# Kernel optimization log

Measured on AMD Instinct MI355X. Metric: run time of the kernel, lower is better.

Reference implementation:

```python
import jax, jax.numpy as jnp
import numpy as np

NEG_SLOPE = 0.2   # LeakyReLU default negative slope (GATv2 + nn.LeakyReLU)
K_NEIGH = 16      # att_args['num_neighs']


def leaky(x):
    return jnp.where(x >= 0, x, NEG_SLOPE * x)


def knn_idx(x_feat, y_feat, k):
    """Per-batch KNN of y in x (feature space). x_feat,y_feat: [B,M,C] -> [B,M,k] local idx into x."""
    d = (jnp.sum(y_feat * y_feat, -1, keepdims=True)
         - 2.0 * jnp.einsum('bmc,bnc->bmn', y_feat, x_feat)
         + jnp.sum(x_feat * x_feat, -1)[:, None, :])   # [B,M,M]
    _, idx = jax.lax.top_k(-d, k)
    return idx


def gatv2_bipartite(x_last, x_past, nbr, Wl, Wr, att_w):
    """Faithful GATv2Conv((last, past), edge_index) with flow='target_to_source',
    heads H, concat=False (mean over heads), bias=False, no self loops.
    x_j = lin_l(x[0]=last) gathered at knn neighbor (col) indices,
    x_i = lin_r(x[1]=past) at query (row) indices; each query has exactly K edges."""
    N, C = x_last.shape
    H = att_w.shape[0]
    xl = (x_last @ Wl).reshape(N, H, C)          # [N,H,C]
    xr = (x_past @ Wr).reshape(N, H, C)          # [N,H,C]
    xlj = xl[nbr]                                 # [N,K,H,C] gathered source msgs
    e = jnp.einsum('nkhc,hc->nkh', leaky(xlj + xr[:, None]), att_w)  # [N,K,H]
    a = jax.nn.softmax(e, axis=1)                 # softmax over each target's K edges
    out = jnp.einsum('nkh,nkhc->nhc', a, xlj)     # [N,H,C]
    return out.mean(axis=1)                       # concat=False -> head mean, [N,C]


def reference(pc_encoded_seq, W1, b1, W2, b2, Wl, Wr, att_w, batch_size, m_points):
    T, N, C = pc_encoded_seq.shape
    B, M = batch_size, m_points
    G = W2.shape[1]
    # node_level_proj (Linear-LeakyReLU-Linear-LeakyReLU) + global_mean_pool per frame
    h = leaky(leaky(pc_encoded_seq @ W1 + b1) @ W2 + b2)      # [T,N,G]
    global_fea = h.reshape(T, B, M, G).mean(axis=2)            # [T,B,G]
    # frame-level ScaledDotProductAttention: q = last frame, k=v = past frames
    q = global_fea[-1][:, None, :]                             # [B,1,G]
    kv = jnp.transpose(global_fea[:-1], (1, 0, 2))             # [B,T-1,G]
    score = jnp.einsum('bqg,btg->bqt', q, kv) / jnp.sqrt(jnp.asarray(G, jnp.float32))
    attn = jax.nn.softmax(score, axis=-1)                      # [B,1,T-1]
    last = pc_encoded_seq[-1]                                  # [N,C]
    lastb = last.reshape(B, M, C)
    offs = (jnp.arange(B) * M)[:, None, None]
    res = []
    for i in range(T - 1):   # small fixed frame count
        past = pc_encoded_seq[i]
        nbr = knn_idx(past.reshape(B, M, C), lastb, K_NEIGH) + offs  # global idx
        out = gatv2_bipartite(last, past, nbr.reshape(N, K_NEIGH), Wl, Wr, att_w)
        res.append(out.reshape(B, M, C))
    res = jnp.stack(res, axis=1)                               # [B,T-1,M,C]
    fw = attn[:, 0, :, None, None]                             # [B,T-1,1,1]
    weighted = jnp.sum(res * fw, axis=1)                       # [B,M,C]
    tm_out = jnp.concatenate([last, weighted.reshape(N, C)], axis=-1)  # [N,2C]
    return tm_out


def setup_inputs() -> dict:
    key = jax.random.key(0)
    ks = jax.random.split(key, 8)
    T, B, M, C, G, H = 5, 4, 4096, 128, 1024, 4
    N = B * M
    s = lambda fan: 1.0 / np.sqrt(fan)
    return {
        'pc_encoded_seq': jax.random.normal(ks[0], (T, N, C), jnp.float32),
        'W1': jax.random.normal(ks[1], (C, 128), jnp.float32) * s(C),
        'b1': jnp.zeros((128,), jnp.float32),
        'W2': jax.random.normal(ks[2], (128, G), jnp.float32) * s(128),
        'b2': jnp.zeros((G,), jnp.float32),
        'Wl': jax.random.normal(ks[3], (C, H * C), jnp.float32) * s(C),
        'Wr': jax.random.normal(ks[4], (C, H * C), jnp.float32) * s(C),
        'att_w': jax.random.normal(ks[5], (H, C), jnp.float32) * s(C),
        'batch_size': B,
        'm_points': M,
    }
```

## Files before the change

### kernel.cpp

```cpp
#include <hip/hip_runtime.h>
#include <hip/hip_bf16.h>
#include <hip/hip_fp16.h>


typedef __bf16 v8bf __attribute__((ext_vector_type(8)));
typedef float  v4f  __attribute__((ext_vector_type(4)));

__device__ __forceinline__ float lrelu(float x) { return fmaxf(x, 0.2f * x); }

__device__ __forceinline__ unsigned short f2bf(float x) {
  __hip_bfloat16 h = __float2bfloat16(x);
  return __builtin_bit_cast(unsigned short, h);
}
__device__ __forceinline__ float bf2f(unsigned short u) {
  unsigned int t = ((unsigned int)u) << 16;
  return __builtin_bit_cast(float, t);
}

#define GLOAD_LDS16(gp, lp)                                                   \
  __builtin_amdgcn_global_load_lds(                                           \
      (const __attribute__((address_space(1))) void*)(gp),                    \
      (__attribute__((address_space(3))) void*)(lp), 16, 0, 0)

#define RBAR() do { __builtin_amdgcn_s_barrier(); asm volatile("" ::: "memory"); } while (0)
#define LWAIT() do { asm volatile("s_waitcnt lgkmcnt(0)" ::: "memory");        \
                     __builtin_amdgcn_sched_barrier(0); } while (0)

template<int EP>
__global__ __launch_bounds__(256, 2)
void nt_mfma(const unsigned short* __restrict__ A, const unsigned short* __restrict__ B,
             const float* __restrict__ aux, void* __restrict__ outv, int K, int ldc)
{
  __shared__ __align__(16) unsigned short smem[3 * 8192];
  const int tid = threadIdx.x;
  const int l = tid & 63;
  const int w = tid >> 6;
  const int wm = w & 1, wn = w >> 1;
  const int m0 = blockIdx.y << 7, n0 = blockIdx.x << 7;
  const int fr = l & 15, quad = l >> 4;
  const int kt = K >> 5;
  const int xq4 = quad ^ ((fr >> 1) & 3);

  const int r0 = tid >> 2;
  const int sw = (tid & 3) ^ ((tid >> 3) & 3);
  const unsigned short* Aa = A + (size_t)(m0 + r0) * K + sw * 8;
  const unsigned short* Ab = Aa + (size_t)64 * K;
  const unsigned short* Ba = B + (size_t)(n0 + r0) * K + sw * 8;
  const unsigned short* Bb = Ba + (size_t)64 * K;

  auto stage = [&](int bi, int ks) {
    unsigned short* As = smem + bi * 8192;
    unsigned short* Bs = As + 4096;
    GLOAD_LDS16(Aa + ks * 32, As + tid * 8);
    GLOAD_LDS16(Ab + ks * 32, As + (tid + 256) * 8);
    GLOAD_LDS16(Ba + ks * 32, Bs + tid * 8);
    GLOAD_LDS16(Bb + ks * 32, Bs + (tid + 256) * 8);
  };

  v4f acc[4][4];
#pragma unroll
  for (int i = 0; i < 4; ++i)
#pragma unroll
    for (int j = 0; j < 4; ++j) acc[i][j] = (v4f){0.f, 0.f, 0.f, 0.f};

  stage(0, 0);
  if (kt > 1) stage(1, 1);
  int cur = 0, pend = (kt > 1) ? 2 : 1, sn = 2;

  for (int ks = 0; ks < kt; ++ks) {
    if (pend == 2) asm volatile("s_waitcnt vmcnt(4)" ::: "memory");
    else           asm volatile("s_waitcnt vmcnt(0)" ::: "memory");
    RBAR();
    int nb = cur + 2; if (nb >= 3) nb -= 3;
    if (sn < kt) { stage(nb, sn); ++sn; } else { --pend; }
    const unsigned short* As = smem + cur * 8192;
    const unsigned short* Bs = As + 4096;
    v8bf af[4], bfr[4];
#pragma unroll
    for (int i = 0; i < 4; ++i)
      af[i] = *(const v8bf*)(As + (wm * 64 + i * 16 + fr) * 32 + xq4 * 8);
#pragma unroll
    for (int j = 0; j < 4; ++j)
      bfr[j] = *(const v8bf*)(Bs + (wn * 64 + j * 16 + fr) * 32 + xq4 * 8);
#pragma unroll
    for (int i = 0; i < 4; ++i)
#pragma unroll
      for (int j = 0; j < 4; ++j)
        acc[i][j] = __builtin_amdgcn_mfma_f32_16x16x32_bf16(af[i], bfr[j], acc[i][j], 0, 0, 0);
    __builtin_amdgcn_sched_barrier(0);
    if (++cur == 3) cur = 0;
  }

  if (EP == 1) {
    unsigned short* O = (unsigned short*)outv;
#pragma unroll
    for (int j = 0; j < 4; ++j) {
      int col = n0 + wn * 64 + j * 16 + fr;
      float bias = aux[col];
#pragma unroll
      for (int i = 0; i < 4; ++i) {
        int row = m0 + wm * 64 + i * 16 + quad * 4;
#pragma unroll
        for (int r = 0; r < 4; ++r)
          O[(size_t)(row + r) * ldc + col] = f2bf(lrelu(acc[i][j][r] + bias));
      }
    }
  } else if (EP == 2) {
    __syncthreads();
    float* red = (float*)smem;
#pragma unroll
    for (int j = 0; j < 4; ++j) {
      int lcol = wn * 64 + j * 16 + fr;
      float bias = aux[n0 + lcol];
      float s = 0.f;
#pragma unroll
      for (int i = 0; i < 4; ++i)
#pragma unroll
        for (int r = 0; r < 4; ++r) s += lrelu(acc[i][j][r] + bias);
      s += __shfl_xor(s, 16);
      s += __shfl_xor(s, 32);
      if (quad == 0) red[w * 128 + lcol] = s;
    }
    __syncthreads();
    if (tid < 128) {
      float s = (tid < 64) ? red[0 * 128 + tid] + red[1 * 128 + tid]
                           : red[2 * 128 + tid] + red[3 * 128 + tid];
      atomicAdd((float*)outv + ((m0 >> 12) << 10) + n0 + tid, s * (1.0f / 4096.0f));
    }
  } else {
    __half* O = (__half*)outv;
#pragma unroll
    for (int j = 0; j < 4; ++j) {
      int col = n0 + wn * 64 + j * 16 + fr;
#pragma unroll
      for (int i = 0; i < 4; ++i) {
        int row = m0 + wm * 64 + i * 16 + quad * 4;
#pragma unroll
        for (int r = 0; r < 4; ++r)
          O[(size_t)(row + r) * ldc + col] = __float2half(acc[i][j][r]);
      }
    }
  }
}

#define TOPN 24
#define TSTR 25
#define FB   16
#define PSTR 17

__global__ __launch_bounds__(256, 2)
void knn_coarse(const unsigned short* __restrict__ seqbf,
                const float* __restrict__ xsq, int* __restrict__ candOut)
{
  __shared__ __align__(16) unsigned short smem[16384];
  __shared__ float topV[128 * TSTR];
  __shared__ int   topI[128 * TSTR];
  __shared__ float pushV[128 * PSTR];
  __shared__ int   pushI[128 * PSTR];
  __shared__ int   cntW[128];

  const int tid = threadIdx.x;
  const int l = tid & 63;
  const int w = tid >> 6;
  const int pair = blockIdx.x >> 5;
  const int rb = blockIdx.x & 31;
  const int f = pair >> 2, b = pair & 3;
  const int m0 = rb << 7;
  const int fr = l & 15, quad = l >> 4;
  const int xq4 = quad ^ ((fr >> 1) & 3);

  const unsigned short* ybase = seqbf + ((size_t)65536 + b * 4096) * 128;
  const unsigned short* xbase = seqbf + ((size_t)(f * 16384 + b * 4096)) * 128;
  const float* xq = xsq + f * 16384 + b * 4096;

  const int r0 = tid >> 2;
  const int sw = (tid & 3) ^ ((tid >> 3) & 3);

#pragma unroll
  for (int kk = 0; kk < 4; ++kk) {
    const unsigned short* Ag = ybase + (size_t)(m0 + r0) * 128 + kk * 32 + sw * 8;
    GLOAD_LDS16(Ag, smem + kk * 4096 + tid * 8);
    GLOAD_LDS16(Ag + 64 * 128, smem + kk * 4096 + (tid + 256) * 8);
  }
  asm volatile("s_waitcnt vmcnt(0)" ::: "memory");
  RBAR();

  v8bf afr[4][2];
#pragma unroll
  for (int kk = 0; kk < 4; ++kk)
#pragma unroll
    for (int i = 0; i < 2; ++i)
      afr[kk][i] = *(const v8bf*)(smem + kk * 4096 + (w * 32 + i * 16 + fr) * 32 + xq4 * 8);
  LWAIT();

  float tauReg = -3.0e38f;
  float ownMin = -3.0e38f;
  int   ownMinPos = 0;
  if (l < 32) {
    const int grow = w * 32 + l;
#pragma unroll
    for (int k = 0; k < TOPN; ++k) { topV[grow * TSTR + k] = -3.0e38f; topI[grow * TSTR + k] = k; }
    cntW[grow] = 0;
  }
  float tc[8];
#pragma unroll
  for (int i = 0; i < 8; ++i) tc[i] = -3.0e38f;

  for (int ct = 0; ct < 32; ++ct) {
    const int n0 = ct << 7;
    RBAR();
    {
      const unsigned short* Bt = xbase + (size_t)(n0 + r0) * 128 + sw * 8;
#pragma unroll
      for (int kk = 0; kk < 4; ++kk) {
        GLOAD_LDS16(Bt + kk * 32, smem + kk * 4096 + tid * 8);
        GLOAD_LDS16(Bt + 64 * 128 + kk * 32, smem + kk * 4096 + (tid + 256) * 8);
      }
    }
    float xsv[8];
#pragma unroll
    for (int j = 0; j < 8; ++j) xsv[j] = xq[n0 + j * 16 + fr];
    asm volatile("s_waitcnt vmcnt(0)" ::: "memory");
    RBAR();

    v4f acc[2][8];
#pragma unroll
    for (int i = 0; i < 2; ++i)
#pragma unroll
      for (int j = 0; j < 8; ++j) acc[i][j] = (v4f){0.f, 0.f, 0.f, 0.f};

#pragma unroll
    for (int ksp = 0; ksp < 4; ++ksp) {
      v8bf bfr[8];
#pragma unroll
      for (int j = 0; j < 8; ++j)
        bfr[j] = *(const v8bf*)(smem + ksp * 4096 + (j * 16 + fr) * 32 + xq4 * 8);
#pragma unroll
      for (int i = 0; i < 2; ++i)
#pragma unroll
        for (int j = 0; j < 8; ++j)
          acc[i][j] = __builtin_amdgcn_mfma_f32_16x16x32_bf16(afr[ksp][i], bfr[j], acc[i][j], 0, 0, 0);
    }

#pragma unroll
    for (int i = 0; i < 2; ++i)
#pragma unroll
      for (int j = 0; j < 8; ++j)
#pragma unroll
        for (int r = 0; r < 4; ++r)
          acc[i][j][r] = 2.f * acc[i][j][r] - xsv[j];

    if (ct == 0) {
#pragma unroll
      for (int i = 0; i < 2; ++i)
#pragma unroll
        for (int r = 0; r < 4; ++r) {
          float t1 = fmaxf(acc[i][0][r], acc[i][1][r]);
          float t2 = fminf(acc[i][0][r], acc[i][1][r]);
#pragma unroll
          for (int j = 2; j < 8; ++j) {
            float v = acc[i][j][r];
            float hi = fmaxf(t1, v);
            t2 = fmaxf(t2, fminf(t1, v));
            t1 = hi;
          }
#pragma unroll
          for (int off = 1; off <= 8; off <<= 1)
            t2 = fminf(t2, __shfl_xor(t2, off));
          tc[i * 4 + r] = t2;
          float tq = __shfl(t2, (((l >> 2) & 3) << 4));
          if (l < 32 && (l >> 4) == i && (l & 3) == r) tauReg = tq;
        }
    }

    unsigned long long pushed = 0ull;
    for (;;) {
#pragma unroll
      for (int i = 0; i < 2; ++i)
#pragma unroll
        for (int r = 0; r < 4; ++r) {
          const float tau = tc[i * 4 + r];
          int mca = 0;
#pragma unroll
          for (int j = 0; j < 8; ++j) {
            const int bit = i * 32 + j * 4 + r;
            if (acc[i][j][r] > tau && !((pushed >> bit) & 1ull)) mca |= (1 << j);
          }
          unsigned long long bal = __ballot(mca != 0);
          if ((bal >> (quad << 4)) & 0xFFFFull) {
            const int lrow = w * 32 + i * 16 + quad * 4 + r;
#pragma unroll
            for (int j = 0; j < 8; ++j)
              if ((mca >> j) & 1) {
                int pos = atomicAdd(&cntW[lrow], 1);
                if (pos < FB) {
                  pushV[lrow * PSTR + pos] = acc[i][j][r];
                  pushI[lrow * PSTR + pos] = n0 + j * 16 + fr;
                  pushed |= (1ull << (i * 32 + j * 4 + r));
                }
              }
          }
        }
      LWAIT();
      bool ov = false;
      if (l < 32) {
        const int grow = w * 32 + l;
        int c = cntW[grow];
        int cc = c < FB ? c : FB;
        for (int q = 0; q < cc; ++q) {
          float v = pushV[grow * PSTR + q];
          if (v > ownMin) {
            topV[grow * TSTR + ownMinPos] = v;
            topI[grow * TSTR + ownMinPos] = pushI[grow * PSTR + q];
            ownMin = topV[grow * TSTR]; ownMinPos = 0;
#pragma unroll
            for (int k = 1; k < TOPN; ++k) {
              float tk = topV[grow * TSTR + k];
              if (tk < ownMin) { ownMin = tk; ownMinPos = k; }
            }
          }
        }
        tauReg = fmaxf(tauReg, ownMin);
        ov = c > FB;
        cntW[grow] = 0;
      }
      LWAIT();
#pragma unroll
      for (int i = 0; i < 2; ++i)
#pragma unroll
        for (int r = 0; r < 4; ++r)
          tc[i * 4 + r] = __shfl(tauReg, i * 16 + quad * 4 + r);
      if (!__any(ov)) break;
    }
  }

  if (l < 32) {
    const int grow = w * 32 + l;
    int* outp = candOut + ((size_t)(f * 16384 + b * 4096 + m0 + grow)) * TOPN;
#pragma unroll
    for (int k = 0; k < TOPN; ++k) outp[k] = topI[grow * TSTR + k];
  }
}

__global__ __launch_bounds__(256)
void knn_rescore(const float* __restrict__ seq, const float* __restrict__ xsq,
                 const int* __restrict__ cand, int* __restrict__ nbrOut)
{
  const int tid = threadIdx.x;
  const int l = tid & 63;
  const int blk = blockIdx.x;
  const int pair = ((blk & 7) << 1) | ((blk >> 3) & 1);
  const int qb = blk >> 4;
  const int f = pair >> 2, b = pair & 3;
  const int qloc = qb * 4 + (tid >> 6);
  const int gq = pair * 4096 + qloc;

  const float2 yv = ((const float2*)(seq + ((size_t)65536 + b * 4096 + qloc) * 128))[l];
  const float* xslice = seq + (size_t)(f * 16384 + (b << 12)) * 128;
  const float* xsqs = xsq + f * 16384 + (b << 12);

  const int myi = cand[(size_t)gq * 24 + (l < 24 ? l : 0)];
  const float xsq_mine = xsqs[myi];

  float2 xv[24];
#pragma unroll
  for (int j = 0; j < 24; ++j) {
    int cj = __shfl(myi, j);
    xv[j] = ((const float2*)(xslice + (size_t)cj * 128))[l];
  }
  float p[24];
#pragma unroll
  for (int j = 0; j < 24; ++j) p[j] = yv.x * xv[j].x + yv.y * xv[j].y;
#pragma unroll
  for (int off = 1; off <= 32; off <<= 1)
#pragma unroll
    for (int j = 0; j < 24; ++j) p[j] += __shfl_xor(p[j], off);

  float myv = -3.0e38f;
#pragma unroll
  for (int j = 0; j < 24; ++j) if (l == j) myv = 2.f * p[j] - xsq_mine;

  int rank = 0;
#pragma unroll
  for (int j = 0; j < 24; ++j) {
    float vj = __shfl(myv, j);
    rank += (vj > myv || (vj == myv && j < l)) ? 1 : 0;
  }
  if (l < 24 && rank < 16)
    nbrOut[(size_t)gq * 16 + rank] = (b << 12) + myi;
}

__global__ __launch_bounds__(256)
void convert_inputs(const float* __restrict__ seq, unsigned short* __restrict__ seqbf,
                    unsigned short* __restrict__ ylay, unsigned short* __restrict__ xlay,
                    float* __restrict__ xsq)
{
  const int tid = threadIdx.x;
  const int row = blockIdx.x * 8 + (tid >> 5);
  const int c4 = tid & 31;
  float4 v = *(const float4*)(seq + (size_t)row * 128 + c4 * 4);
  ushort4 hi, lo;
  hi.x = f2bf(v.x); lo.x = f2bf(v.x - bf2f(hi.x));
  hi.y = f2bf(v.y); lo.y = f2bf(v.y - bf2f(hi.y));
  hi.z = f2bf(v.z); lo.z = f2bf(v.z - bf2f(hi.z));
  hi.w = f2bf(v.w); lo.w = f2bf(v.w - bf2f(hi.w));
  *(ushort4*)(seqbf + (size_t)row * 128 + c4 * 4) = hi;
  float ss = v.x * v.x + v.y * v.y + v.z * v.z + v.w * v.w;
#pragma unroll
  for (int off = 16; off; off >>= 1) ss += __shfl_xor(ss, off);
  if (row < 65536) {
    unsigned short* p = xlay + (size_t)row * 384 + c4 * 4;
    *(ushort4*)(p) = hi; *(ushort4*)(p + 128) = lo; *(ushort4*)(p + 256) = hi;
    if (c4 == 0) xsq[row] = ss;
  } else {
    unsigned short* p = ylay + (size_t)(row - 65536) * 384 + c4 * 4;
    *(ushort4*)(p) = hi; *(ushort4*)(p + 128) = hi; *(ushort4*)(p + 256) = lo;
  }
}

__global__ __launch_bounds__(256)
void convert_weights(const float* __restrict__ W1, const float* __restrict__ W2,
                     const float* __restrict__ Wl, const float* __restrict__ Wr,
                     const float* __restrict__ aw,
                     unsigned short* __restrict__ W1t, unsigned short* __restrict__ W2t,
                     unsigned short* __restrict__ Wlv, unsigned short* __restrict__ Wrv,
                     __half* __restrict__ awh)
{
  int idx = blockIdx.x * 256 + threadIdx.x;
  if (idx < 16384) {
    int n = idx >> 7, k = idx & 127;
    W1t[idx] = f2bf(W1[k * 128 + n]);
  } else if (idx < 147456) {
    int i = idx - 16384; int n = i >> 7, k = i & 127;
    W2t[i] = f2bf(W2[k * 1024 + n]);
  } else if (idx < 344064) {
    int i = idx - 147456; int n = i / 384, k = i % 384;
    int s = k >> 7, kk = k & 127;
    float wv = Wl[kk * 512 + n];
    unsigned short h = f2bf(wv);
    Wlv[i] = (s == 1) ? f2bf(wv - bf2f(h)) : h;
  } else if (idx < 540672) {
    int i = idx - 344064; int n = i / 384, k = i % 384;
    int s = k >> 7, kk = k & 127;
    float wv = Wr[kk * 512 + n];
    unsigned short h = f2bf(wv);
    Wrv[i] = (s == 2) ? f2bf(wv - bf2f(h)) : h;
  } else if (idx < 541184) {
    int i = idx - 540672;
    awh[i] = __float2half(aw[i]);
  }
}

__global__ __launch_bounds__(1024)
void temporal_attn(const float* __restrict__ gfea, float* __restrict__ attnw)
{
  const int tid = threadIdx.x;
  const int w = tid >> 6, l = tid & 63;
  const int b = w >> 2, i = w & 3;
  const float* q  = gfea + (16 + b) * 1024;
  const float* kv = gfea + (i * 4 + b) * 1024;
  float p = 0.f;
  for (int g = l; g < 1024; g += 64) p += q[g] * kv[g];
#pragma unroll
  for (int off = 32; off; off >>= 1) p += __shfl_xor(p, off);
  __shared__ float sc[16];
  if (l == 0) sc[w] = p * 0.03125f;
  __syncthreads();
  if (tid < 4) {
    float v0 = sc[tid * 4 + 0], v1 = sc[tid * 4 + 1];
    float v2 = sc[tid * 4 + 2], v3 = sc[tid * 4 + 3];
    float mm = fmaxf(fmaxf(v0, v1), fmaxf(v2, v3));
    v0 = __expf(v0 - mm); v1 = __expf(v1 - mm);
    v2 = __expf(v2 - mm); v3 = __expf(v3 - mm);
    float inv = 1.f / (v0 + v1 + v2 + v3);
    attnw[tid * 4 + 0] = v0 * inv;
    attnw[tid * 4 + 1] = v1 * inv;
    attnw[tid * 4 + 2] = v2 * inv;
    attnw[tid * 4 + 3] = v3 * inv;
  }
}

__global__ __launch_bounds__(256)
void gat6(const __half* __restrict__ xlh, const __half* __restrict__ xrh,
          const int* __restrict__ nbr, const __half* __restrict__ awh,
          const float* __restrict__ attnw, float* __restrict__ wgt4)
{
  const int tid = threadIdx.x;
  const int l = tid & 63;
  const int blk = blockIdx.x;
  const int r8 = blk & 7;
  const int b = r8 >> 1;
  const int g = ((blk >> 3) << 1) | (r8 & 1);
  const int f = g >> 10;
  const int n4 = g & 1023;
  const int qid = f * 16384 + b * 4096 + n4 * 4 + (tid >> 6);
  const int h = l >> 4, cp = l & 15;
  const float fw = attnw[b * 4 + f] * 0.25f;

  const int jl = nbr[qid * 16 + (l & 15)];
  const __half* xbase = xlh + h * 128 + cp * 8;

  const __half2* xrp = (const __half2*)(xrh + (size_t)qid * 512 + h * 128 + cp * 8);
  float2 xr0 = __half22float2(xrp[0]), xr1 = __half22float2(xrp[1]);
  float2 xr2 = __half22float2(xrp[2]), xr3 = __half22float2(xrp[3]);
  const __half2* awp = (const __half2*)(awh + h * 128 + cp * 8);
  float2 aw0 = __half22float2(awp[0]), aw1 = __half22float2(awp[1]);
  float2 aw2 = __half22float2(awp[2]), aw3 = __half22float2(awp[3]);

  float m = -3.0e38f, s = 0.f;
  float o[8];
#pragma unroll
  for (int c = 0; c < 8; ++c) o[c] = 0.f;

  for (int ch = 0; ch < 2; ++ch) {
    float4 xv[8];
#pragma unroll
    for (int k = 0; k < 8; ++k) {
      int j = __shfl(jl, ch * 8 + k);
      xv[k] = *(const float4*)(xbase + (size_t)j * 512);
    }
    float e[8];
#pragma unroll
    for (int k = 0; k < 8; ++k) {
      const __half2* hp = (const __half2*)&xv[k];
      float2 x0 = __half22float2(hp[0]), x1 = __half22float2(hp[1]);
      float2 x2 = __half22float2(hp[2]), x3 = __half22float2(hp[3]);
      float p = 0.f;
      p += lrelu(x0.x + xr0.x) * aw0.x + lrelu(x0.y + xr0.y) * aw0.y;
      p += lrelu(x1.x + xr1.x) * aw1.x + lrelu(x1.y + xr1.y) * aw1.y;
      p += lrelu(x2.x + xr2.x) * aw2.x + lrelu(x2.y + xr2.y) * aw2.y;
      p += lrelu(x3.x + xr3.x) * aw3.x + lrelu(x3.y + xr3.y) * aw3.y;
      p += __shfl_xor(p, 1);
      p += __shfl_xor(p, 2);
      p += __shfl_xor(p, 4);
      p += __shfl_xor(p, 8);
      e[k] = p;
    }
    float mc = e[0];
#pragma unroll
    for (int k = 1; k < 8; ++k) mc = fmaxf(mc, e[k]);
    float mn = fmaxf(m, mc);
    float cr = __expf(m - mn);
    s *= cr;
#pragma unroll
    for (int c = 0; c < 8; ++c) o[c] *= cr;
#pragma unroll
    for (int k = 0; k < 8; ++k) {
      float a = __expf(e[k] - mn);
      s += a;
      const __half2* hp = (const __half2*)&xv[k];
      float2 f0 = __half22float2(hp[0]);
      float2 f1 = __half22float2(hp[1]);
      float2 f2 = __half22float2(hp[2]);
      float2 f3 = __half22float2(hp[3]);
      o[0] += a * f0.x; o[1] += a * f0.y;
      o[2] += a * f1.x; o[3] += a * f1.y;
      o[4] += a * f2.x; o[5] += a * f2.y;
      o[6] += a * f3.x; o[7] += a * f3.y;
    }
    m = mn;
  }

  const float sc = fw / s;
#pragma unroll
  for (int c = 0; c < 8; ++c) {
    float t = o[c] * sc;
    t += __shfl_xor(t, 16);
    t += __shfl_xor(t, 32);
    o[c] = t;
  }
  if (l < 16) {
    float* wp = wgt4 + (size_t)qid * 128 + l * 8;
    *(float4*)(wp)     = make_float4(o[0], o[1], o[2], o[3]);
    *(float4*)(wp + 4) = make_float4(o[4], o[5], o[6], o[7]);
  }
}

__global__ __launch_bounds__(256)
void finalize2(const float* __restrict__ last, const float* __restrict__ wgt4,
               float* __restrict__ out)
{
  int idx = blockIdx.x * 256 + threadIdx.x;
  int n = idx >> 6, q = idx & 63;
  float4 v;
  if (q < 32) {
    v = *(const float4*)(last + (size_t)n * 128 + 4 * q);
  } else {
    int c = (q - 32) * 4;
    v = make_float4(0.f, 0.f, 0.f, 0.f);
#pragma unroll
    for (int f = 0; f < 4; ++f) {
      float4 t = *(const float4*)(wgt4 + ((size_t)f * 16384 + n) * 128 + c);
      v.x += t.x; v.y += t.y; v.z += t.z; v.w += t.w;
    }
  }
  *(float4*)(out + (size_t)n * 256 + 4 * q) = v;
}

extern "C" void kernel_launch(void* const* d_in, const int* in_sizes, int n_in,
                              void* d_out, int out_size, void* d_ws, size_t ws_size,
                              hipStream_t stream)
{
  (void)in_sizes; (void)n_in; (void)out_size; (void)ws_size;
  const float* seq = (const float*)d_in[0];
  const float* W1  = (const float*)d_in[1];
  const float* b1  = (const float*)d_in[2];
  const float* W2  = (const float*)d_in[3];
  const float* b2  = (const float*)d_in[4];
  const float* Wl  = (const float*)d_in[5];
  const float* Wr  = (const float*)d_in[6];
  const float* aw  = (const float*)d_in[7];
  float* out = (float*)d_out;

  float* ws = (float*)d_ws;
  __half* xrh          = (__half*)ws;
  unsigned short* seqbf = (unsigned short*)(ws + 16777216);
  unsigned short* h1bf  = (unsigned short*)(ws + 22020096);
  int* cand24           = (int*)(ws + 22020096);
  __half* xlh           = (__half*)(ws + 22020096);
  unsigned short* ylay  = (unsigned short*)(ws + 27262976);
  unsigned short* xlay  = (unsigned short*)(ws + 30408704);
  float* wgt4           = ws + 30408704;
  float* gfea           = ws + 42991616;
  float* attn           = gfea + 20480;
  float* xsq            = attn + 16;
  int*   nbr            = (int*)(xsq + 65536);
  unsigned short* W1t   = (unsigned short*)(nbr + 1048576);
  unsigned short* W2t   = W1t + 16384;
  unsigned short* Wlv   = W2t + 131072;
  unsigned short* Wrv   = Wlv + 196608;
  __half* awh           = (__half*)(Wrv + 196608);

  (void)hipMemsetAsync(gfea, 0, 20480 * sizeof(float), stream);

  convert_inputs<<<10240, 256, 0, stream>>>(seq, seqbf, ylay, xlay, xsq);
  convert_weights<<<2114, 256, 0, stream>>>(W1, W2, Wl, Wr, aw, W1t, W2t, Wlv, Wrv, awh);

  nt_mfma<1><<<dim3(1, 640), 256, 0, stream>>>(seqbf, W1t, b1, h1bf, 128, 128);
  nt_mfma<2><<<dim3(8, 640), 256, 0, stream>>>(h1bf, W2t, b2, gfea, 128, 0);
  temporal_attn<<<1, 1024, 0, stream>>>(gfea, attn);

  knn_coarse<<<512, 256, 0, stream>>>(seqbf, xsq, cand24);
  knn_rescore<<<16384, 256, 0, stream>>>(seq, xsq, cand24, nbr);

  nt_mfma<3><<<dim3(4, 128), 256, 0, stream>>>(ylay, Wlv, nullptr, xlh, 384, 512);
  nt_mfma<3><<<dim3(4, 512), 256, 0, stream>>>(xlay, Wrv, nullptr, xrh, 384, 512);

  gat6<<<16384, 256, 0, stream>>>(xlh, xrh, nbr, awh, attn, wgt4);

  finalize2<<<4096, 256, 0, stream>>>(seq + (size_t)4 * 16384 * 128, wgt4, out);
}
```

Baseline: 916.4 us.

## Shrink KNN coarse tiles to 64 rows, reduce candidates to 20, vectorize rescore

The coarse KNN kernel now processes 64 query rows per block instead of 128, with A fragments loaded straight from global memory and the B tile staged in two K-halves through a smaller LDS buffer. That cuts LDS and register use so four blocks can run per CU, and the launch doubles to 1024 blocks with pair-interleaved block ordering. The candidate list shrinks from 24 to 20 and the push buffer from 16 to 10. The rescore kernel now uses float4 loads split across 8 lanes per candidate plus an LDS rank step. Fewer candidates increase the risk of missing true neighbours near ties after bf16 coarse scoring, and the split B load adds extra barriers.

```diff
diff --git a/kernel.cpp b/kernel.cpp
--- a/kernel.cpp
+++ b/kernel.cpp
@@ -143,29 +143,30 @@
   }
 }
 
-#define TOPN 24
-#define TSTR 25
-#define FB   16
-#define PSTR 17
-
-__global__ __launch_bounds__(256, 2)
+#define TOPN 20
+#define TSTR 21
+#define FB   10
+#define PSTR 11
+
+__global__ __launch_bounds__(256, 4)
 void knn_coarse(const unsigned short* __restrict__ seqbf,
                 const float* __restrict__ xsq, int* __restrict__ candOut)
 {
-  __shared__ __align__(16) unsigned short smem[16384];
-  __shared__ float topV[128 * TSTR];
-  __shared__ int   topI[128 * TSTR];
-  __shared__ float pushV[128 * PSTR];
-  __shared__ int   pushI[128 * PSTR];
-  __shared__ int   cntW[128];
+  __shared__ __align__(16) unsigned short bsm[8192];
+  __shared__ float topV[64 * TSTR];
+  __shared__ int   topI[64 * TSTR];
+  __shared__ float pushV[64 * PSTR];
+  __shared__ int   pushI[64 * PSTR];
+  __shared__ int   cntW[64];
 
   const int tid = threadIdx.x;
   const int l = tid & 63;
   const int w = tid >> 6;
-  const int pair = blockIdx.x >> 5;
-  const int rb = blockIdx.x & 31;
+  const int blk = blockIdx.x;
+  const int pair = ((blk & 7) << 1) | ((blk >> 3) & 1);
+  const int rb = blk >> 4;
   const int f = pair >> 2, b = pair & 3;
-  const int m0 = rb << 7;
+  const int m0 = rb << 6;
   const int fr = l & 15, quad = l >> 4;
   const int xq4 = quad ^ ((fr >> 1) & 3);
 
@@ -176,135 +177,131 @@
   const int r0 = tid >> 2;
   const int sw = (tid & 3) ^ ((tid >> 3) & 3);
 
-#pragma unroll
-  for (int kk = 0; kk < 4; ++kk) {
-    const unsigned short* Ag = ybase + (size_t)(m0 + r0) * 128 + kk * 32 + sw * 8;
-    GLOAD_LDS16(Ag, smem + kk * 4096 + tid * 8);
-    GLOAD_LDS16(Ag + 64 * 128, smem + kk * 4096 + (tid + 256) * 8);
-  }
-  asm volatile("s_waitcnt vmcnt(0)" ::: "memory");
-  RBAR();
-
-  v8bf afr[4][2];
-#pragma unroll
-  for (int kk = 0; kk < 4; ++kk)
-#pragma unroll
-    for (int i = 0; i < 2; ++i)
-      afr[kk][i] = *(const v8bf*)(smem + kk * 4096 + (w * 32 + i * 16 + fr) * 32 + xq4 * 8);
-  LWAIT();
+  v8bf afr[4];
+#pragma unroll
+  for (int ksp = 0; ksp < 4; ++ksp)
+    afr[ksp] = *(const v8bf*)(ybase + (size_t)(m0 + w * 16 + fr) * 128 + ksp * 32 + quad * 8);
 
   float tauReg = -3.0e38f;
   float ownMin = -3.0e38f;
   int   ownMinPos = 0;
-  if (l < 32) {
-    const int grow = w * 32 + l;
+  if (l < 16) {
+    const int grow = w * 16 + l;
 #pragma unroll
     for (int k = 0; k < TOPN; ++k) { topV[grow * TSTR + k] = -3.0e38f; topI[grow * TSTR + k] = k; }
     cntW[grow] = 0;
   }
-  float tc[8];
-#pragma unroll
-  for (int i = 0; i < 8; ++i) tc[i] = -3.0e38f;
+  float tc[4];
+#pragma unroll
+  for (int r = 0; r < 4; ++r) tc[r] = -3.0e38f;
+  LWAIT();
 
   for (int ct = 0; ct < 32; ++ct) {
     const int n0 = ct << 7;
+    const unsigned short* Bt = xbase + (size_t)(n0 + r0) * 128 + sw * 8;
+
     RBAR();
-    {
-      const unsigned short* Bt = xbase + (size_t)(n0 + r0) * 128 + sw * 8;
-#pragma unroll
-      for (int kk = 0; kk < 4; ++kk) {
-        GLOAD_LDS16(Bt + kk * 32, smem + kk * 4096 + tid * 8);
-        GLOAD_LDS16(Bt + 64 * 128 + kk * 32, smem + kk * 4096 + (tid + 256) * 8);
-      }
-    }
+    GLOAD_LDS16(Bt, bsm + tid * 8);
+    GLOAD_LDS16(Bt + 64 * 128, bsm + (tid + 256) * 8);
+    GLOAD_LDS16(Bt + 32, bsm + 4096 + tid * 8);
+    GLOAD_LDS16(Bt + 64 * 128 + 32, bsm + 4096 + (tid + 256) * 8);
     float xsv[8];
 #pragma unroll
     for (int j = 0; j < 8; ++j) xsv[j] = xq[n0 + j * 16 + fr];
     asm volatile("s_waitcnt vmcnt(0)" ::: "memory");
     RBAR();
 
-    v4f acc[2][8];
-#pragma unroll
-    for (int i = 0; i < 2; ++i)
-#pragma unroll
-      for (int j = 0; j < 8; ++j) acc[i][j] = (v4f){0.f, 0.f, 0.f, 0.f};
-
-#pragma unroll
-    for (int ksp = 0; ksp < 4; ++ksp) {
+    v4f acc[8];
+#pragma unroll
+    for (int j = 0; j < 8; ++j) acc[j] = (v4f){0.f, 0.f, 0.f, 0.f};
+
+#pragma unroll
+    for (int ksp = 0; ksp < 2; ++ksp) {
       v8bf bfr[8];
 #pragma unroll
       for (int j = 0; j < 8; ++j)
-        bfr[j] = *(const v8bf*)(smem + ksp * 4096 + (j * 16 + fr) * 32 + xq4 * 8);
-#pragma unroll
-      for (int i = 0; i < 2; ++i)
-#pragma unroll
-        for (int j = 0; j < 8; ++j)
-          acc[i][j] = __builtin_amdgcn_mfma_f32_16x16x32_bf16(afr[ksp][i], bfr[j], acc[i][j], 0, 0, 0);
-    }
-
-#pragma unroll
-    for (int i = 0; i < 2; ++i)
+        bfr[j] = *(const v8bf*)(bsm + ksp * 4096 + (j * 16 + fr) * 32 + xq4 * 8);
 #pragma unroll
       for (int j = 0; j < 8; ++j)
-#pragma unroll
-        for (int r = 0; r < 4; ++r)
-          acc[i][j][r] = 2.f * acc[i][j][r] - xsv[j];
+        acc[j] = __builtin_amdgcn_mfma_f32_16x16x32_bf16(afr[ksp], bfr[j], acc[j], 0, 0, 0);
+    }
+    LWAIT();
+    RBAR();
+
+    GLOAD_LDS16(Bt + 2 * 32, bsm + tid * 8);
+    GLOAD_LDS16(Bt + 64 * 128 + 2 * 32, bsm + (tid + 256) * 8);
+    GLOAD_LDS16(Bt + 3 * 32, bsm + 4096 + tid * 8);
+    GLOAD_LDS16(Bt + 64 * 128 + 3 * 32, bsm + 4096 + (tid + 256) * 8);
+    asm volatile("s_waitcnt vmcnt(0)" ::: "memory");
+    RBAR();
+
+#pragma unroll
+    for (int ksp = 0; ksp < 2; ++ksp) {
+      v8bf bfr[8];
+#pragma unroll
+      for (int j = 0; j < 8; ++j)
+        bfr[j] = *(const v8bf*)(bsm + ksp * 4096 + (j * 16 + fr) * 32 + xq4 * 8);
+#pragma unroll
+      for (int j = 0; j < 8; ++j)
+        acc[j] = __builtin_amdgcn_mfma_f32_16x16x32_bf16(afr[2 + ksp], bfr[j], acc[j], 0, 0, 0);
+    }
+
+#pragma unroll
+    for (int j = 0; j < 8; ++j)
+#pragma unroll
+      for (int r = 0; r < 4; ++r)
+        acc[j][r] = 2.f * acc[j][r] - xsv[j];
 
     if (ct == 0) {
 #pragma unroll
-      for (int i = 0; i < 2; ++i)
-#pragma unroll
-        for (int r = 0; r < 4; ++r) {
-          float t1 = fmaxf(acc[i][0][r], acc[i][1][r]);
-          float t2 = fminf(acc[i][0][r], acc[i][1][r]);
-#pragma unroll
-          for (int j = 2; j < 8; ++j) {
-            float v = acc[i][j][r];
-            float hi = fmaxf(t1, v);
-            t2 = fmaxf(t2, fminf(t1, v));
-            t1 = hi;
-          }
-#pragma unroll
-          for (int off = 1; off <= 8; off <<= 1)
-            t2 = fminf(t2, __shfl_xor(t2, off));
-          tc[i * 4 + r] = t2;
-          float tq = __shfl(t2, (((l >> 2) & 3) << 4));
-          if (l < 32 && (l >> 4) == i && (l & 3) == r) tauReg = tq;
+      for (int r = 0; r < 4; ++r) {
+        float t1 = fmaxf(acc[0][r], acc[1][r]);
+        float t2 = fminf(acc[0][r], acc[1][r]);
+#pragma unroll
+        for (int j = 2; j < 8; ++j) {
+          float v = acc[j][r];
+          float hi = fmaxf(t1, v);
+          t2 = fmaxf(t2, fminf(t1, v));
+          t1 = hi;
         }
-    }
-
-    unsigned long long pushed = 0ull;
+#pragma unroll
+        for (int off = 1; off <= 8; off <<= 1)
+          t2 = fminf(t2, __shfl_xor(t2, off));
+        tc[r] = t2;
+        float tq = __shfl(t2, (l >> 2) << 4);
+        if (l < 16 && (l & 3) == r) tauReg = tq;
+      }
+    }
+
+    unsigned int pushed = 0u;
     for (;;) {
 #pragma unroll
-      for (int i = 0; i < 2; ++i)
-#pragma unroll
-        for (int r = 0; r < 4; ++r) {
-          const float tau = tc[i * 4 + r];
-          int mca = 0;
-#pragma unroll
-          for (int j = 0; j < 8; ++j) {
-            const int bit = i * 32 + j * 4 + r;
-            if (acc[i][j][r] > tau && !((pushed >> bit) & 1ull)) mca |= (1 << j);
-          }
-          unsigned long long bal = __ballot(mca != 0);
-          if ((bal >> (quad << 4)) & 0xFFFFull) {
-            const int lrow = w * 32 + i * 16 + quad * 4 + r;
-#pragma unroll
-            for (int j = 0; j < 8; ++j)
-              if ((mca >> j) & 1) {
-                int pos = atomicAdd(&cntW[lrow], 1);
-                if (pos < FB) {
-                  pushV[lrow * PSTR + pos] = acc[i][j][r];
-                  pushI[lrow * PSTR + pos] = n0 + j * 16 + fr;
-                  pushed |= (1ull << (i * 32 + j * 4 + r));
-                }
+      for (int r = 0; r < 4; ++r) {
+        const float tau = tc[r];
+        int mca = 0;
+#pragma unroll
+        for (int j = 0; j < 8; ++j) {
+          const int bit = j * 4 + r;
+          if (acc[j][r] > tau && !((pushed >> bit) & 1u)) mca |= (1 << j);
+        }
+        if (__any(mca != 0)) {
+          const int lrow = w * 16 + quad * 4 + r;
+#pragma unroll
+          for (int j = 0; j < 8; ++j)
+            if ((mca >> j) & 1) {
+              int pos = atomicAdd(&cntW[lrow], 1);
+              if (pos < FB) {
+                pushV[lrow * PSTR + pos] = acc[j][r];
+                pushI[lrow * PSTR + pos] = n0 + j * 16 + fr;
+                pushed |= (1u << (j * 4 + r));
               }
-          }
+            }
         }
+      }
       LWAIT();
       bool ov = false;
-      if (l < 32) {
-        const int grow = w * 32 + l;
+      if (l < 16) {
+        const int grow = w * 16 + l;
         int c = cntW[grow];
         int cc = c < FB ? c : FB;
         for (int q = 0; q < cc; ++q) {
@@ -326,16 +323,14 @@
       }
       LWAIT();
 #pragma unroll
-      for (int i = 0; i < 2; ++i)
-#pragma unroll
-        for (int r = 0; r < 4; ++r)
-          tc[i * 4 + r] = __shfl(tauReg, i * 16 + quad * 4 + r);
+      for (int r = 0; r < 4; ++r)
+        tc[r] = __shfl(tauReg, quad * 4 + r);
       if (!__any(ov)) break;
     }
   }
 
-  if (l < 32) {
-    const int grow = w * 32 + l;
+  if (l < 16) {
+    const int grow = w * 16 + l;
     int* outp = candOut + ((size_t)(f * 16384 + b * 4096 + m0 + grow)) * TOPN;
 #pragma unroll
     for (int k = 0; k < TOPN; ++k) outp[k] = topI[grow * TSTR + k];
@@ -346,48 +341,59 @@
 void knn_rescore(const float* __restrict__ seq, const float* __restrict__ xsq,
                  const int* __restrict__ cand, int* __restrict__ nbrOut)
 {
+  __shared__ float sc[4][20];
   const int tid = threadIdx.x;
   const int l = tid & 63;
+  const int wq = tid >> 6;
   const int blk = blockIdx.x;
   const int pair = ((blk & 7) << 1) | ((blk >> 3) & 1);
   const int qb = blk >> 4;
   const int f = pair >> 2, b = pair & 3;
-  const int qloc = qb * 4 + (tid >> 6);
+  const int qloc = qb * 4 + wq;
   const int gq = pair * 4096 + qloc;
 
-  const float2 yv = ((const float2*)(seq + ((size_t)65536 + b * 4096 + qloc) * 128))[l];
+  const int c8 = l & 7;
+  const int h  = l >> 3;
+  const float* yrow = seq + ((size_t)65536 + b * 4096 + qloc) * 128 + h * 16;
+  float4 y0 = *(const float4*)(yrow);
+  float4 y1 = *(const float4*)(yrow + 4);
+  float4 y2 = *(const float4*)(yrow + 8);
+  float4 y3 = *(const float4*)(yrow + 12);
   const float* xslice = seq + (size_t)(f * 16384 + (b << 12)) * 128;
   const float* xsqs = xsq + f * 16384 + (b << 12);
-
-  const int myi = cand[(size_t)gq * 24 + (l < 24 ? l : 0)];
-  const float xsq_mine = xsqs[myi];
-
-  float2 xv[24];
-#pragma unroll
-  for (int j = 0; j < 24; ++j) {
-    int cj = __shfl(myi, j);
-    xv[j] = ((const float2*)(xslice + (size_t)cj * 128))[l];
-  }
-  float p[24];
-#pragma unroll
-  for (int j = 0; j < 24; ++j) p[j] = yv.x * xv[j].x + yv.y * xv[j].y;
-#pragma unroll
-  for (int off = 1; off <= 32; off <<= 1)
-#pragma unroll
-    for (int j = 0; j < 24; ++j) p[j] += __shfl_xor(p[j], off);
-
-  float myv = -3.0e38f;
-#pragma unroll
-  for (int j = 0; j < 24; ++j) if (l == j) myv = 2.f * p[j] - xsq_mine;
-
-  int rank = 0;
-#pragma unroll
-  for (int j = 0; j < 24; ++j) {
-    float vj = __shfl(myv, j);
-    rank += (vj > myv || (vj == myv && j < l)) ? 1 : 0;
-  }
-  if (l < 24 && rank < 16)
-    nbrOut[(size_t)gq * 16 + rank] = (b << 12) + myi;
+  const int* cq = cand + (size_t)gq * 20;
+
+#pragma unroll
+  for (int rd = 0; rd < 3; ++rd) {
+    int cr = rd * 8 + c8;
+    int crc = cr < 20 ? cr : 0;
+    int cj = cq[crc];
+    const float* xr = xslice + (size_t)cj * 128 + h * 16;
+    float4 x0 = *(const float4*)(xr);
+    float4 x1 = *(const float4*)(xr + 4);
+    float4 x2 = *(const float4*)(xr + 8);
+    float4 x3 = *(const float4*)(xr + 12);
+    float p = y0.x * x0.x + y0.y * x0.y + y0.z * x0.z + y0.w * x0.w
+            + y1.x * x1.x + y1.y * x1.y + y1.z * x1.z + y1.w * x1.w
+            + y2.x * x2.x + y2.y * x2.y + y2.z * x2.z + y2.w * x2.w
+            + y3.x * x3.x + y3.y * x3.y + y3.z * x3.z + y3.w * x3.w;
+    p += __shfl_xor(p, 8);
+    p += __shfl_xor(p, 16);
+    p += __shfl_xor(p, 32);
+    if (h == 0 && cr < 20) sc[wq][cr] = 2.f * p - xsqs[cj];
+  }
+  LWAIT();
+  if (l < 20) {
+    float myv = sc[wq][l];
+    int rank = 0;
+#pragma unroll
+    for (int j = 0; j < 20; ++j) {
+      float vj = sc[wq][j];
+      rank += (vj > myv || (vj == myv && j < l)) ? 1 : 0;
+    }
+    if (rank < 16)
+      nbrOut[(size_t)gq * 16 + rank] = (b << 12) + cq[l];
+  }
 }
 
 __global__ __launch_bounds__(256)
@@ -616,7 +622,7 @@
   __half* xrh          = (__half*)ws;
   unsigned short* seqbf = (unsigned short*)(ws + 16777216);
   unsigned short* h1bf  = (unsigned short*)(ws + 22020096);
-  int* cand24           = (int*)(ws + 22020096);
+  int* cand20           = (int*)(ws + 22020096);
   __half* xlh           = (__half*)(ws + 22020096);
   unsigned short* ylay  = (unsigned short*)(ws + 27262976);
   unsigned short* xlay  = (unsigned short*)(ws + 30408704);
@@ -640,8 +646,8 @@
   nt_mfma<2><<<dim3(8, 640), 256, 0, stream>>>(h1bf, W2t, b2, gfea, 128, 0);
   temporal_attn<<<1, 1024, 0, stream>>>(gfea, attn);
 
-  knn_coarse<<<512, 256, 0, stream>>>(seqbf, xsq, cand24);
-  knn_rescore<<<16384, 256, 0, stream>>>(seq, xsq, cand24, nbr);
+  knn_coarse<<<1024, 256, 0, stream>>>(seqbf, xsq, cand20);
+  knn_rescore<<<16384, 256, 0, stream>>>(seq, xsq, cand20, nbr);
 
   nt_mfma<3><<<dim3(4, 128), 256, 0, stream>>>(ylay, Wlv, nullptr, xlh, 384, 512);
   nt_mfma<3><<<dim3(4, 512), 256, 0, stream>>>(xlay, Wrv, nullptr, xrh, 384, 512);
```

After: 782.3 us. -14.6%, faster.
